# Performance work log

Hardware: AMD Instinct MI355X
Metric: run time of the kernel (lower is better)

Reference implementation:

```python
import jax, jax.numpy as jnp
import numpy as np

PC = (-51.2, -51.2, -5.0, 51.2, 51.2, 3.0)
BEV_H, BEV_W, BEV_Z = 50, 50, 4
NCAM, NUM_HEADS = 6, 8
EPS = 1e-5


def _layer_norm(x, g, b):
    m = jnp.mean(x, -1, keepdims=True)
    v = jnp.mean((x - m) ** 2, -1, keepdims=True)
    return (x - m) / jnp.sqrt(v + 1e-5) * g + b


def _grid_sample(imgs, pts):
    # imgs: (B,C,H,W); pts: (B,N,2) normalized coords; bilinear,
    # align_corners=False, zero padding (matches F.grid_sample defaults).
    B, C, H, W = imgs.shape
    def one(img, p):
        x = ((p[:, 0] + 1.0) * W - 1.0) * 0.5
        y = ((p[:, 1] + 1.0) * H - 1.0) * 0.5
        x0 = jnp.floor(x); y0 = jnp.floor(y)
        wx = x - x0; wy = y - y0
        def g(xi, yi):
            ok = (xi >= 0) & (xi < W) & (yi >= 0) & (yi < H)
            v = img[:, jnp.clip(yi, 0, H - 1).astype(jnp.int32),
                       jnp.clip(xi, 0, W - 1).astype(jnp.int32)]
            return v * ok[None, :]
        return (g(x0, y0) * (1 - wx) * (1 - wy) + g(x0 + 1, y0) * wx * (1 - wy)
                + g(x0, y0 + 1) * (1 - wx) * wy + g(x0 + 1, y0 + 1) * wx * wy)
    return jax.vmap(one)(imgs, pts)  # (B,C,N)


def _mha(q, kv, inW, inb, outW, outb):
    # torch nn.MultiheadAttention (batch_first)
    C = q.shape[-1]; d = C // NUM_HEADS
    B, Nq = q.shape[:2]; Nk = kv.shape[1]
    Q = q @ inW[:C].T + inb[:C]
    K = kv @ inW[C:2 * C].T + inb[C:2 * C]
    V = kv @ inW[2 * C:].T + inb[2 * C:]
    Qh = Q.reshape(B, Nq, NUM_HEADS, d).transpose(0, 2, 1, 3)
    Kh = K.reshape(B, Nk, NUM_HEADS, d).transpose(0, 2, 1, 3)
    Vh = V.reshape(B, Nk, NUM_HEADS, d).transpose(0, 2, 1, 3)
    s = jnp.einsum('bhqd,bhkd->bhqk', Qh, Kh) / float(np.sqrt(d))
    a = jax.nn.softmax(s, axis=-1)
    o = jnp.einsum('bhqk,bhkd->bhqd', a, Vh).transpose(0, 2, 1, 3).reshape(B, Nq, C)
    return o @ outW.T + outb


def _warp_prev(prev_bev, ego_motion):
    B, N, C = prev_bev.shape
    sp = prev_bev.transpose(0, 2, 1).reshape(B, C, BEV_H, BEV_W)
    tx = ego_motion[:, 0, 3]; ty = ego_motion[:, 1, 3]
    yaw = jnp.arctan2(ego_motion[:, 1, 0], ego_motion[:, 0, 0])
    dx = tx / ((PC[3] - PC[0]) / BEV_W) * 2.0 / BEV_W
    dy = ty / ((PC[4] - PC[1]) / BEV_H) * 2.0 / BEV_H
    c = jnp.cos(yaw); s = jnp.sin(yaw)
    theta = jnp.stack([jnp.stack([c, -s, dx], -1),
                       jnp.stack([s, c, dy], -1)], axis=1)  # (B,2,3)
    # F.affine_grid, align_corners=False: output-pixel-center base grid
    xs = (2.0 * jnp.arange(BEV_W) + 1.0) / BEV_W - 1.0
    ys = (2.0 * jnp.arange(BEV_H) + 1.0) / BEV_H - 1.0
    gx, gy = jnp.meshgrid(xs, ys)  # (H,W) each
    base = jnp.stack([gx, gy, jnp.ones_like(gx)], -1)  # (H,W,3)
    grid = jnp.einsum('bij,hwj->bhwi', theta, base).reshape(B, -1, 2)
    out = _grid_sample(sp, grid)  # (B,C,N)
    return out.transpose(0, 2, 1)


def _reference_points(B):
    ys = (jnp.arange(BEV_H, dtype=jnp.float32) + 0.5) / BEV_H
    xs = (jnp.arange(BEV_W, dtype=jnp.float32) + 0.5) / BEV_W
    ry, rx = jnp.meshgrid(ys, xs, indexing='ij')
    rx = rx.reshape(-1); ry = ry.reshape(-1)
    zs = (jnp.arange(BEV_Z, dtype=jnp.float32) + 0.5) / BEV_Z
    N = BEV_H * BEV_W
    ref = jnp.stack([jnp.broadcast_to(rx[:, None], (N, BEV_Z)),
                     jnp.broadcast_to(ry[:, None], (N, BEV_Z)),
                     jnp.broadcast_to(zs[None, :], (N, BEV_Z))], -1)
    return jnp.broadcast_to(ref[None], (B, N, BEV_Z, 3))  # (B,Nq,Z,3)


def _point_sampling(ref, img_feats, lidar2img):
    B, Nq, Zb, _ = ref.shape
    _, Ncam, C, Hf, Wf = img_feats.shape
    x = ref[..., 0] * (PC[3] - PC[0]) + PC[0]
    y = ref[..., 1] * (PC[4] - PC[1]) + PC[1]
    z = ref[..., 2] * (PC[5] - PC[2]) + PC[2]
    pts = jnp.stack([x, y, z, jnp.ones_like(x)], -1).reshape(B, 1, Nq * Zb, 4)
    pts = jnp.broadcast_to(pts, (B, Ncam, Nq * Zb, 4))
    cam = jnp.einsum('bnij,bnpj->bnpi', lidar2img, pts)
    depth = cam[..., 2]
    xy = cam[..., 0:2] / jnp.clip(depth, EPS)[..., None]
    gx = (xy[..., 0] / (Wf - 1) - 0.5) * 2.0
    gy = (xy[..., 1] / (Hf - 1) - 0.5) * 2.0
    valid = ((depth > EPS) & (gx > -1.0) & (gx < 1.0)
             & (gy > -1.0) & (gy < 1.0))  # (B,Ncam,Nq*Zb)
    grid = jnp.stack([gx, gy], -1).reshape(B * Ncam, Nq * Zb, 2)
    samp = _grid_sample(img_feats.reshape(B * Ncam, C, Hf, Wf), grid)
    samp = samp.reshape(B, Ncam, C, Nq, Zb) * valid.reshape(B, Ncam, 1, Nq, Zb)
    return jnp.nan_to_num(samp)


def _forward(query, prev_bev, img_feats, ego_motion, lidar2img,
             attn_w_W, attn_w_b, sca_out_W, sca_out_b,
             in_proj_W, in_proj_b, mha_out_W, mha_out_b,
             norm1_g, norm1_b, ffn_W1, ffn_b1, ffn_W2, ffn_b2,
             norm2_g, norm2_b):
    B, Nq, C = query.shape
    # Temporal self-attention with warped previous BEV
    aligned = _warp_prev(prev_bev, ego_motion)
    kv = jnp.concatenate([query, aligned], axis=1)
    attn = _mha(query, kv, in_proj_W, in_proj_b, mha_out_W, mha_out_b)
    q = _layer_norm(query + attn, norm1_g, norm1_b)
    # Spatial cross attention
    ref = _reference_points(B)
    samp = _point_sampling(ref, img_feats, lidar2img)  # (B,Ncam,C,Nq,Z)
    w = (q @ attn_w_W.T + attn_w_b).reshape(B, Nq, NCAM * BEV_Z)
    w = jax.nn.softmax(w, axis=-1).reshape(B, Nq, NCAM, BEV_Z)
    agg = jnp.einsum('bncqz,bqnz->bqc', samp, w)
    q = agg @ sca_out_W.T + sca_out_b + q
    # FFN (Linear -> ReLU -> Linear -> LayerNorm), residual outside
    h = jax.nn.relu(q @ ffn_W1.T + ffn_b1) @ ffn_W2.T + ffn_b2
    return q + _layer_norm(h, norm2_g, norm2_b)


def setup_inputs() -> dict:
    key = jax.random.key(0)
    ks = jax.random.split(key, 16)
    B, Nq, C, Hf, Wf = 1, BEV_H * BEV_W, 256, 28, 50
    s = 0.02
    d = {
        'query': jax.random.normal(ks[0], (B, Nq, C), jnp.float32),
        'prev_bev': jax.random.normal(ks[1], (B, Nq, C), jnp.float32),
        'img_feats': jax.random.normal(ks[2], (B, NCAM, C, Hf, Wf), jnp.float32),
        'ego_motion': jax.random.normal(ks[3], (B, 4, 4), jnp.float32),
        'lidar2img': jax.random.normal(ks[4], (B, NCAM, 4, 4), jnp.float32),
        'attn_w_W': jax.random.normal(ks[5], (NCAM * BEV_Z, C), jnp.float32) * s,
        'attn_w_b': jnp.zeros((NCAM * BEV_Z,), jnp.float32),
        'sca_out_W': jax.random.normal(ks[6], (C, C), jnp.float32) * s,
        'sca_out_b': jnp.zeros((C,), jnp.float32),
        'in_proj_W': jax.random.normal(ks[7], (3 * C, C), jnp.float32) * s,
        'in_proj_b': jnp.zeros((3 * C,), jnp.float32),
        'mha_out_W': jax.random.normal(ks[8], (C, C), jnp.float32) * s,
        'mha_out_b': jnp.zeros((C,), jnp.float32),
        'norm1_g': jnp.ones((C,), jnp.float32),
        'norm1_b': jnp.zeros((C,), jnp.float32),
        'ffn_W1': jax.random.normal(ks[9], (2 * C, C), jnp.float32) * s,
        'ffn_b1': jnp.zeros((2 * C,), jnp.float32),
        'ffn_W2': jax.random.normal(ks[10], (C, 2 * C), jnp.float32) * s,
        'ffn_b2': jnp.zeros((C,), jnp.float32),
        'norm2_g': jnp.ones((C,), jnp.float32),
        'norm2_b': jnp.zeros((C,), jnp.float32),
    }
    return d


def reference(query, prev_bev, img_feats, ego_motion, lidar2img,
              attn_w_W, attn_w_b, sca_out_W, sca_out_b,
              in_proj_W, in_proj_b, mha_out_W, mha_out_b,
              norm1_g, norm1_b, ffn_W1, ffn_b1, ffn_W2, ffn_b2,
              norm2_g, norm2_b):
    return _forward(query, prev_bev, img_feats, ego_motion, lidar2img,
                    attn_w_W, attn_w_b, sca_out_W, sca_out_b,
                    in_proj_W, in_proj_b, mha_out_W, mha_out_b,
                    norm1_g, norm1_b, ffn_W1, ffn_b1, ffn_W2, ffn_b2,
                    norm2_g, norm2_b)
```

## Files before the change

kernel.cpp:

```cpp
#include <hip/hip_runtime.h>
#include <hip/hip_bf16.h>
#include <math.h>

#define NQ   2500
#define CDIM 256
#define NKV  5000
#define NH   8
#define DH   32
#define SPLITS 10
#define KPS   500
#define FULLT 7
#define TILES 8
#define TAILNK 52

typedef __attribute__((ext_vector_type(8))) short bf16x8;
typedef __attribute__((ext_vector_type(4))) short short4v;
typedef __attribute__((ext_vector_type(4))) float f32x4;

#define MFMA __builtin_amdgcn_mfma_f32_16x16x32_bf16

__device__ __forceinline__ short f2bf(float f) {
  union { float f; unsigned u; } v; v.f = f;
  unsigned r = v.u + 0x7FFFu + ((v.u >> 16) & 1u);
  return (short)(r >> 16);
}
__device__ __forceinline__ float bf2f(unsigned short s) {
  union { unsigned u; float f; } x; x.u = ((unsigned)s) << 16; return x.f;
}
__device__ __forceinline__ unsigned pk_trunc(float a, float b) {
  union { float f; unsigned u; } x, y; x.f = a; y.f = b;
  return (y.u & 0xFFFF0000u) | (x.u >> 16);
}
__device__ __forceinline__ unsigned cvt_pk_bf16(float a, float b) {
  unsigned r;
  asm("v_cvt_pk_bf16_f32 %0, %1, %2" : "=v"(r) : "v"(a), "v"(b));
  return r;
}
__device__ __forceinline__ float exp2_fast(float x) {
  float r; asm("v_exp_f32 %0, %1" : "=v"(r) : "v"(x)); return r;
}

__global__ __launch_bounds__(256) void k_build_kv(
    const float* __restrict__ query, const float* __restrict__ prev,
    const float* __restrict__ ego, float* __restrict__ kv)
{
  int row = blockIdx.x, c = threadIdx.x;
  if (row < NQ) { kv[(size_t)row*CDIM + c] = query[(size_t)row*CDIM + c]; return; }
  int n = row - NQ;
  float txm = ego[3], tym = ego[7];
  float yaw = atan2f(ego[4], ego[0]);
  float cs = cosf(yaw), sn = sinf(yaw);
  float dx = txm * (1.f/51.2f), dy = tym * (1.f/51.2f);
  int i = n / 50, j = n % 50;
  float gx = (2.f*j + 1.f)*(1.f/50.f) - 1.f;
  float gy = (2.f*i + 1.f)*(1.f/50.f) - 1.f;
  float px = cs*gx - sn*gy + dx;
  float py = sn*gx + cs*gy + dy;
  float xf = ((px + 1.f)*50.f - 1.f)*0.5f;
  float yf = ((py + 1.f)*50.f - 1.f)*0.5f;
  float x0f = floorf(xf), y0f = floorf(yf);
  int x0 = (int)x0f, y0 = (int)y0f;
  float wx = xf - x0f, wy = yf - y0f;
  float v00 = (x0  >=0 && x0  <50 && y0  >=0 && y0  <50) ? prev[((size_t)(y0*50+x0      ))*CDIM + c] : 0.f;
  float v10 = (x0+1>=0 && x0+1<50 && y0  >=0 && y0  <50) ? prev[((size_t)(y0*50+x0+1    ))*CDIM + c] : 0.f;
  float v01 = (x0  >=0 && x0  <50 && y0+1>=0 && y0+1<50) ? prev[((size_t)((y0+1)*50+x0  ))*CDIM + c] : 0.f;
  float v11 = (x0+1>=0 && x0+1<50 && y0+1>=0 && y0+1<50) ? prev[((size_t)((y0+1)*50+x0+1))*CDIM + c] : 0.f;
  float v = (v00*(1.f-wx) + v10*wx)*(1.f-wy) + (v01*(1.f-wx) + v11*wx)*wy;
  kv[(size_t)row*CDIM + c] = v;
}

__global__ __launch_bounds__(256) void k_prep_w(
    const float* __restrict__ inW, const float* __restrict__ moW,
    const float* __restrict__ scaW, const float* __restrict__ fW1,
    const float* __restrict__ fW2, short* __restrict__ wf)
{
  const int id = blockIdx.x*256 + threadIdx.x;
  if (id >= 73728) return;
  const int s = id*8;
  const float* src; int off, K, obase;
  if      (s < 65536)  { src = inW;          off = s;          K = 256; obase = 0; }
  else if (s < 131072) { src = inW + 65536;  off = s - 65536;  K = 256; obase = 65536; }
  else if (s < 196608) { src = inW + 131072; off = s - 131072; K = 256; obase = 131072; }
  else if (s < 262144) { src = moW;          off = s - 196608; K = 256; obase = 196608; }
  else if (s < 327680) { src = scaW;         off = s - 262144; K = 256; obase = 262144; }
  else if (s < 458752) { src = fW1;          off = s - 327680; K = 256; obase = 327680; }
  else                 { src = fW2;          off = s - 458752; K = 512; obase = 458752; }
  const int n = off / K, k = off - n*K;
  short4v lo, hi;
  #pragma unroll
  for (int j = 0; j < 4; ++j) { lo[j] = f2bf(src[off+j]); hi[j] = f2bf(src[off+4+j]); }
  short* dst = wf + obase + (size_t)((n>>4)*(K>>3) + (k>>3))*128 + (n&15)*8;
  *(short4v*)dst = lo;
  *(short4v*)(dst+4) = hi;
}

__global__ __launch_bounds__(256) void k_repack_v(
    const short* __restrict__ VbfT, short* __restrict__ Vf)
{
  const int idx = blockIdx.x*256 + threadIdx.x;
  const int j    = idx & 7;
  const int lane = (idx >> 3) & 63;
  const int i    = (idx >> 9) & 1;
  const int kt2  = (idx >> 10) & 1;
  const int t    = (idx >> 11) & 7;
  const int h    = (idx >> 14) & 7;
  const int sp   = idx >> 17;
  const int gg = lane >> 4, cc = lane & 15;
  const int ko32 = ((j >> 2) << 4) | (gg << 2) | (j & 3);
  const int kin = t*64 + kt2*32 + ko32;
  const int d = i*16 + cc;
  short v = 0;
  if (kin < KPS) v = VbfT[(size_t)(h*32 + d)*NKV + sp*KPS + kin];
  Vf[idx] = v;
}

__global__ __launch_bounds__(256) void k_transpose_img(
    const float* __restrict__ img, unsigned short* __restrict__ imgT)
{
  int b = blockIdx.x;
  int n = b / 28, y = b % 28;
  int c = threadIdx.x;
  for (int x = 0; x < 50; ++x)
    imgT[((size_t)((n*28 + y)*50 + x))*CDIM + c] =
      (unsigned short)f2bf(img[((size_t)(n*CDIM + c)*28 + y)*50 + x]);
}

__global__ __launch_bounds__(256) void k_gemm(
    const float* __restrict__ A, const short* __restrict__ Wf,
    const float* __restrict__ bias, const float* __restrict__ res,
    float* __restrict__ C, short* __restrict__ Cb,
    int M, int N, int K, int relu, int mode, float scale)
{
  __shared__ short Abf[8][33][8];
  const int tid = threadIdx.x;
  const int lane = tid & 63, wid = tid >> 6;
  const int wm = wid >> 1, wn = wid & 1;
  const int g = lane >> 4, c = lane & 15;
  const int m0 = blockIdx.y << 5, n0 = blockIdx.x << 6;
  const int srow = tid >> 3, skq = tid & 7;
  const int kb8 = K >> 3;
  const short* wfa = Wf + (size_t)((n0 + wn*32) >> 4)      * kb8 * 128 + c*8;
  const short* wfb = Wf + (size_t)(((n0 + wn*32) >> 4) + 1) * kb8 * 128 + c*8;
  f32x4 acc0 = {0.f,0.f,0.f,0.f}, acc1 = acc0;
  const float4 z4 = make_float4(0.f,0.f,0.f,0.f);
  for (int k0 = 0; k0 < K; k0 += 64) {
    float4 fa0 = z4, fa1 = z4;
    if (m0 + srow < M) {
      const float* ap = A + (size_t)(m0+srow)*K + k0 + skq*8;
      fa0 = *(const float4*)ap; fa1 = *(const float4*)(ap+4);
    }
    __syncthreads();
    union { unsigned u[4]; bf16x8 v; } pa;
    pa.u[0] = cvt_pk_bf16(fa0.x, fa0.y);  pa.u[1] = cvt_pk_bf16(fa0.z, fa0.w);
    pa.u[2] = cvt_pk_bf16(fa1.x, fa1.y);  pa.u[3] = cvt_pk_bf16(fa1.z, fa1.w);
    *(bf16x8*)&Abf[skq][srow][0] = pa.v;
    __syncthreads();
    #pragma unroll
    for (int s = 0; s < 2; ++s) {
      const int kq = (k0 >> 3) + s*4 + g;
      const bf16x8 fA  = *(const bf16x8*)&Abf[s*4+g][wm*16 + c][0];
      const bf16x8 fW0 = *(const bf16x8*)(wfa + (size_t)kq*128);
      const bf16x8 fW1 = *(const bf16x8*)(wfb + (size_t)kq*128);
      acc0 = MFMA(fA, fW0, acc0, 0,0,0);
      acc1 = MFMA(fA, fW1, acc1, 0,0,0);
    }
  }
  const int nc0 = n0 + wn*32 + c, nc1 = nc0 + 16;
  const float b0v = bias[nc0], b1v = bias[nc1];
  #pragma unroll
  for (int r = 0; r < 4; ++r) {
    const int m = m0 + wm*16 + g*4 + r;
    if (m >= M) continue;
    float v0 = acc0[r] + b0v;
    float v1 = acc1[r] + b1v;
    if (mode == 0) {
      if (res) { v0 += res[(size_t)m*N + nc0]; v1 += res[(size_t)m*N + nc1]; }
      if (relu) { v0 = fmaxf(v0, 0.f); v1 = fmaxf(v1, 0.f); }
      C[(size_t)m*N + nc0] = v0;
      C[(size_t)m*N + nc1] = v1;
    } else if (mode == 1) {
      Cb[(size_t)m*N + nc0] = f2bf(v0*scale);
      Cb[(size_t)m*N + nc1] = f2bf(v1*scale);
    } else {
      Cb[(size_t)nc0*M + m] = f2bf(v0);
      Cb[(size_t)nc1*M + m] = f2bf(v1);
    }
  }
}

__device__ __forceinline__ void softmax_pv(
    f32x4 s0, f32x4 s1, f32x4 s2, f32x4 s3, bool tail, int g,
    float& m, float& l, f32x4& oA, f32x4& oB,
    bf16x8 A0lo, bf16x8 A0hi, bf16x8 A1lo, bf16x8 A1hi)
{
  float sv[16];
  #pragma unroll
  for (int r=0;r<4;++r){ sv[r]=s0[r]; sv[4+r]=s1[r]; sv[8+r]=s2[r]; sv[12+r]=s3[r]; }
  if (tail) {
    #pragma unroll
    for (int i=0;i<16;++i) {
      const int kl = (i>>2)*16 + g*4 + (i&3);
      if (kl >= TAILNK) sv[i] = -1e30f;
    }
  }
  float mx = fmaxf(fmaxf(fmaxf(sv[0],sv[1]),fmaxf(sv[2],sv[3])),
                   fmaxf(fmaxf(sv[4],sv[5]),fmaxf(sv[6],sv[7])));
  mx = fmaxf(mx, fmaxf(fmaxf(fmaxf(sv[8],sv[9]),fmaxf(sv[10],sv[11])),
                       fmaxf(fmaxf(sv[12],sv[13]),fmaxf(sv[14],sv[15]))));
  if (!__all(mx <= m + 8.f)) {
    float mm = fmaxf(mx, __shfl_xor(mx, 16));
    mm = fmaxf(mm, __shfl_xor(mm, 32));
    const float mn = fmaxf(m, mm);
    const float scl = exp2_fast(m - mn);
    m = mn;
    l *= scl;
    #pragma unroll
    for (int r=0;r<4;++r){ oA[r]*=scl; oB[r]*=scl; }
  }
  float p[16]; float ps = 0.f;
  #pragma unroll
  for (int i=0;i<16;++i){ p[i] = exp2_fast(sv[i]-m); ps += p[i]; }
  l += ps;
  union { unsigned u[4]; bf16x8 v; } b0, b1;
  #pragma unroll
  for (int i=0;i<4;++i) {
    b0.u[i] = pk_trunc(p[2*i],   p[2*i+1]);
    b1.u[i] = pk_trunc(p[8+2*i], p[8+2*i+1]);
  }
  oA = MFMA(A0lo, b0.v, oA, 0,0,0);
  oA = MFMA(A0hi, b1.v, oA, 0,0,0);
  oB = MFMA(A1lo, b0.v, oB, 0,0,0);
  oB = MFMA(A1hi, b1.v, oB, 0,0,0);
}

__global__ __launch_bounds__(64) void k_flash5(
    const short* __restrict__ Qbf, const short* __restrict__ Kbf,
    const short* __restrict__ Vf, short* __restrict__ opart,
    float* __restrict__ mlp)
{
  const int lane = threadIdx.x;
  const int g = lane >> 4, c = lane & 15;
  const int flat = blockIdx.x;
  const int p  = flat % 80;
  const int qb = flat / 80;
  const int h  = p & 7;
  const int sp = p >> 3;
  const int q0 = qb * 32;
  const int qa  = min(q0 +      c, NQ-1);
  const int qb2 = min(q0 + 16 + c, NQ-1);
  const bf16x8 qf0 = *(const bf16x8*)(Qbf + (size_t)qa *CDIM + h*DH + g*8);
  const bf16x8 qf1 = *(const bf16x8*)(Qbf + (size_t)qb2*CDIM + h*DH + g*8);
  const int kbase = sp*KPS;
  const size_t doff = (size_t)h*DH + g*8;
  const short* kbp = Kbf + (size_t)(kbase + c)*CDIM + doff;
  const short* vfp = Vf + (size_t)(sp*NH + h)*(TILES*2048) + lane*8;
  const f32x4 z = {0.f,0.f,0.f,0.f};
  f32x4 o00 = z, o01 = z, o10 = z, o11 = z;
  float m0v = -INFINITY, l0 = 0.f, m1v = -INFINITY, l1 = 0.f;

  bf16x8 kc0 = *(const bf16x8*)(kbp);
  bf16x8 kc1 = *(const bf16x8*)(kbp + (size_t)16*CDIM);
  bf16x8 kc2 = *(const bf16x8*)(kbp + (size_t)32*CDIM);
  bf16x8 kc3 = *(const bf16x8*)(kbp + (size_t)48*CDIM);

  #pragma unroll
  for (int t = 0; t < FULLT; ++t) {
    const int kt = t*64;
    const f32x4 s00 = MFMA(kc0, qf0, z, 0,0,0);
    const f32x4 s01 = MFMA(kc1, qf0, z, 0,0,0);
    const f32x4 s02 = MFMA(kc2, qf0, z, 0,0,0);
    const f32x4 s03 = MFMA(kc3, qf0, z, 0,0,0);
    const f32x4 s10 = MFMA(kc0, qf1, z, 0,0,0);
    const f32x4 s11 = MFMA(kc1, qf1, z, 0,0,0);
    const f32x4 s12 = MFMA(kc2, qf1, z, 0,0,0);
    const f32x4 s13 = MFMA(kc3, qf1, z, 0,0,0);
    if (t+1 < FULLT) {
      kc0 = *(const bf16x8*)(kbp + (size_t)(kt+64)*CDIM);
      kc1 = *(const bf16x8*)(kbp + (size_t)(kt+80)*CDIM);
      kc2 = *(const bf16x8*)(kbp + (size_t)(kt+96)*CDIM);
      kc3 = *(const bf16x8*)(kbp + (size_t)(kt+112)*CDIM);
    }
    const short* vt = vfp + (size_t)t*2048;
    const bf16x8 A0lo = *(const bf16x8*)(vt       );
    const bf16x8 A1lo = *(const bf16x8*)(vt +  512);
    const bf16x8 A0hi = *(const bf16x8*)(vt + 1024);
    const bf16x8 A1hi = *(const bf16x8*)(vt + 1536);
    softmax_pv(s00,s01,s02,s03, false, g, m0v, l0, o00, o01, A0lo, A0hi, A1lo, A1hi);
    softmax_pv(s10,s11,s12,s13, false, g, m1v, l1, o10, o11, A0lo, A0hi, A1lo, A1hi);
  }
  {
    const int kt = FULLT*64;
    const int ka0 = min(kbase + kt +      c, NKV-1);
    const int ka1 = min(kbase + kt + 16 + c, NKV-1);
    const int ka2 = min(kbase + kt + 32 + c, NKV-1);
    const int ka3 = min(kbase + kt + 48 + c, NKV-1);
    const bf16x8 kf0 = *(const bf16x8*)(Kbf + (size_t)ka0*CDIM + doff);
    const bf16x8 kf1 = *(const bf16x8*)(Kbf + (size_t)ka1*CDIM + doff);
    const bf16x8 kf2 = *(const bf16x8*)(Kbf + (size_t)ka2*CDIM + doff);
    const bf16x8 kf3 = *(const bf16x8*)(Kbf + (size_t)ka3*CDIM + doff);
    const f32x4 s00 = MFMA(kf0, qf0, z, 0,0,0);
    const f32x4 s01 = MFMA(kf1, qf0, z, 0,0,0);
    const f32x4 s02 = MFMA(kf2, qf0, z, 0,0,0);
    const f32x4 s03 = MFMA(kf3, qf0, z, 0,0,0);
    const f32x4 s10 = MFMA(kf0, qf1, z, 0,0,0);
    const f32x4 s11 = MFMA(kf1, qf1, z, 0,0,0);
    const f32x4 s12 = MFMA(kf2, qf1, z, 0,0,0);
    const f32x4 s13 = MFMA(kf3, qf1, z, 0,0,0);
    const short* vt = vfp + (size_t)FULLT*2048;
    const bf16x8 A0lo = *(const bf16x8*)(vt       );
    const bf16x8 A1lo = *(const bf16x8*)(vt +  512);
    const bf16x8 A0hi = *(const bf16x8*)(vt + 1024);
    const bf16x8 A1hi = *(const bf16x8*)(vt + 1536);
    softmax_pv(s00,s01,s02,s03, true, g, m0v, l0, o00, o01, A0lo, A0hi, A1lo, A1hi);
    softmax_pv(s10,s11,s12,s13, true, g, m1v, l1, o10, o11, A0lo, A0hi, A1lo, A1hi);
  }
  l0 += __shfl_xor(l0, 16); l0 += __shfl_xor(l0, 32);
  l1 += __shfl_xor(l1, 16); l1 += __shfl_xor(l1, 32);

  const size_t ob0 = (size_t)(sp*NH + h)*NQ;
  const int qw0 = q0 + c;
  if (qw0 < NQ) {
    const size_t b = (ob0 + qw0)*DH;
    #pragma unroll
    for (int r=0;r<4;++r) {
      opart[b +      g*4 + r] = f2bf(o00[r]);
      opart[b + 16 + g*4 + r] = f2bf(o01[r]);
    }
    if (g == 0) { mlp[(ob0 + qw0)*2] = m0v; mlp[(ob0 + qw0)*2+1] = l0; }
  }
  const int qw1 = q0 + 16 + c;
  if (qw1 < NQ) {
    const size_t b = (ob0 + qw1)*DH;
    #pragma unroll
    for (int r=0;r<4;++r) {
      opart[b +      g*4 + r] = f2bf(o10[r]);
      opart[b + 16 + g*4 + r] = f2bf(o11[r]);
    }
    if (g == 0) { mlp[(ob0 + qw1)*2] = m1v; mlp[(ob0 + qw1)*2+1] = l1; }
  }
}

__global__ __launch_bounds__(256) void k_combine(
    const short* __restrict__ opart, const float* __restrict__ mlp,
    float* __restrict__ attn)
{
  const int q = blockIdx.x, t = threadIdx.x;
  const int h = t >> 5, d = t & 31;
  float ms[SPLITS], ls[SPLITS];
  float mstar = -INFINITY;
  #pragma unroll
  for (int s = 0; s < SPLITS; ++s) {
    size_t b = (size_t)(s*NH + h)*NQ + q;
    ms[s] = mlp[b*2]; ls[s] = mlp[b*2+1];
    mstar = fmaxf(mstar, ms[s]);
  }
  float num = 0.f, den = 0.f;
  #pragma unroll
  for (int s = 0; s < SPLITS; ++s) {
    float e = exp2_fast(ms[s] - mstar);
    size_t b = (size_t)(s*NH + h)*NQ + q;
    num += bf2f((unsigned short)opart[b*DH + d])*e;
    den += ls[s]*e;
  }
  attn[(size_t)q*CDIM + t] = num/den;
}

__global__ __launch_bounds__(256) void k_ln(
    const float* __restrict__ x, const float* __restrict__ g,
    const float* __restrict__ b, const float* __restrict__ post_res,
    float* __restrict__ out)
{
  const int row = blockIdx.x, c = threadIdx.x;
  const size_t idx = (size_t)row*CDIM + c;
  const float v = x[idx];
  __shared__ float red[4];
  float s = v;
  #pragma unroll
  for (int m = 1; m < 64; m <<= 1) s += __shfl_xor(s, m);
  if ((c & 63) == 0) red[c >> 6] = s;
  __syncthreads();
  const float mean = (red[0]+red[1]+red[2]+red[3]) * (1.f/256.f);
  const float dv = v - mean;
  __syncthreads();
  float s2 = dv*dv;
  #pragma unroll
  for (int m = 1; m < 64; m <<= 1) s2 += __shfl_xor(s2, m);
  if ((c & 63) == 0) red[c >> 6] = s2;
  __syncthreads();
  const float var = (red[0]+red[1]+red[2]+red[3]) * (1.f/256.f);
  float o = dv * rsqrtf(var + 1e-5f) * g[c] + b[c];
  if (post_res) o += post_res[idx];
  out[idx] = o;
}

__global__ __launch_bounds__(256) void k_sample_agg(
    const float* __restrict__ q1, const unsigned short* __restrict__ imgT,
    const float* __restrict__ l2i, const float* __restrict__ awW,
    const float* __restrict__ awb, float* __restrict__ agg)
{
  const int q = blockIdx.x, tid = threadIdx.x;
  __shared__ float qrow[256];
  __shared__ float wl[24];
  __shared__ float fwx[24], fwy[24];
  __shared__ int iv[24], ix[24], iy[24];
  qrow[tid] = q1[(size_t)q*CDIM + tid];
  __syncthreads();
  if (tid < 192) {
    const int e = tid >> 3, s2 = tid & 7;
    float acc = 0.f;
    for (int c = s2; c < 256; c += 8) acc += qrow[c]*awW[e*256 + c];
    acc += __shfl_xor(acc,1);
    acc += __shfl_xor(acc,2);
    acc += __shfl_xor(acc,4);
    if (s2 == 0) wl[e] = acc + awb[e];
  }
  if (tid < 24) {
    const int e = tid, n = e >> 2, z = e & 3;
    const int iyq = q / 50, jxq = q % 50;
    const float rx = (jxq + 0.5f)*(1.f/50.f);
    const float ry = (iyq + 0.5f)*(1.f/50.f);
    const float rz = (z + 0.5f)*0.25f;
    const float X = rx*102.4f - 51.2f;
    const float Y = ry*102.4f - 51.2f;
    const float Z = rz*8.f - 5.f;
    const float* L = l2i + n*16;
    const float cx = L[0]*X + L[1]*Y + L[2]*Z  + L[3];
    const float cy = L[4]*X + L[5]*Y + L[6]*Z  + L[7];
    const float cd = L[8]*X + L[9]*Y + L[10]*Z + L[11];
    const float dn = fmaxf(cd, 1e-5f);
    const float u = cx/dn, vv = cy/dn;
    const float gx = (u*(1.f/49.f) - 0.5f)*2.f;
    const float gy = (vv*(1.f/27.f) - 0.5f)*2.f;
    const int ok = (cd > 1e-5f) && (gx > -1.f) && (gx < 1.f) && (gy > -1.f) && (gy < 1.f);
    const float xf = ((gx + 1.f)*50.f - 1.f)*0.5f;
    const float yf = ((gy + 1.f)*28.f - 1.f)*0.5f;
    const float x0f = floorf(xf), y0f = floorf(yf);
    iv[e] = ok; ix[e] = (int)x0f; iy[e] = (int)y0f;
    fwx[e] = xf - x0f; fwy[e] = yf - y0f;
  }
  __syncthreads();
  float mx = -INFINITY;
  #pragma unroll
  for (int e = 0; e < 24; ++e) mx = fmaxf(mx, wl[e]);
  float se = 0.f;
  #pragma unroll
  for (int e = 0; e < 24; ++e) se += __expf(wl[e]-mx);
  const float inv = 1.f/se;
  const int c = tid;
  float acc = 0.f;
  #pragma unroll
  for (int e = 0; e < 24; ++e) {
    if (!iv[e]) continue;
    const float w = __expf(wl[e]-mx)*inv;
    const int n = e >> 2;
    const int x0 = ix[e], y0 = iy[e];
    const float wx = fwx[e], wy = fwy[e];
    const size_t base = (size_t)(n*28)*50;
    float v00 = (x0  >=0 && x0  <50 && y0  >=0 && y0  <28) ? bf2f(imgT[((base + (size_t)y0*50     + x0  ))*CDIM + c]) : 0.f;
    float v10 = (x0+1>=0 && x0+1<50 && y0  >=0 && y0  <28) ? bf2f(imgT[((base + (size_t)y0*50     + x0+1))*CDIM + c]) : 0.f;
    float v01 = (x0  >=0 && x0  <50 && y0+1>=0 && y0+1<28) ? bf2f(imgT[((base + (size_t)(y0+1)*50 + x0  ))*CDIM + c]) : 0.f;
    float v11 = (x0+1>=0 && x0+1<50 && y0+1>=0 && y0+1<28) ? bf2f(imgT[((base + (size_t)(y0+1)*50 + x0+1))*CDIM + c]) : 0.f;
    acc += w * ((v00*(1.f-wx) + v10*wx)*(1.f-wy) + (v01*(1.f-wx) + v11*wx)*wy);
  }
  agg[(size_t)q*CDIM + c] = acc;
}

extern "C" void kernel_launch(void* const* d_in, const int* in_sizes, int n_in,
                              void* d_out, int out_size, void* d_ws, size_t ws_size,
                              hipStream_t stream)
{
  const float* query = (const float*)d_in[0];
  const float* prev  = (const float*)d_in[1];
  const float* img   = (const float*)d_in[2];
  const float* ego   = (const float*)d_in[3];
  const float* l2i   = (const float*)d_in[4];
  const float* awW   = (const float*)d_in[5];
  const float* awb   = (const float*)d_in[6];
  const float* scab  = (const float*)d_in[8];
  const float* inb   = (const float*)d_in[10];
  const float* mob   = (const float*)d_in[12];
  const float* n1g   = (const float*)d_in[13];
  const float* n1b   = (const float*)d_in[14];
  const float* fb1   = (const float*)d_in[16];
  const float* fb2   = (const float*)d_in[18];
  const float* n2g   = (const float*)d_in[19];
  const float* n2b   = (const float*)d_in[20];
  float* out = (float*)d_out;
  float* ws  = (float*)d_ws;

  float* kv    = ws;
  short* Qbf   = (short*)(ws + 1280000);
  short* Kbf   = (short*)(ws + 1600000);
  short* VbfT  = (short*)(ws + 2240000);
  short* Vf    = (short*)(ws + 2880000);
  short* opart = (short*)(ws + 3535360);
  float* mlp   = ws + 6735360;
  short* wf    = (short*)(ws + 7135360);
  unsigned short* imgT = (unsigned short*)(ws + 7430272);
  float* attn  = ws;
  float* tmp1  = ws +  640000;
  float* q1    = ws + 1280000;
  float* aggb  = ws + 1920000;
  float* q2    = ws + 2560000;
  float* hbuf  = ws + 3200000;
  float* h2    = ws + 4480000;

  const float qscale = 0.2550727452794943f;

  k_build_kv<<<NKV, 256, 0, stream>>>(query, prev, ego, kv);
  k_prep_w<<<288, 256, 0, stream>>>((const float*)d_in[9], (const float*)d_in[11],
                                    (const float*)d_in[7], (const float*)d_in[15],
                                    (const float*)d_in[17], wf);
  k_transpose_img<<<6*28, 256, 0, stream>>>(img, imgT);
  k_gemm<<<dim3(4,79),  256, 0, stream>>>(kv, wf,          inb,     nullptr, nullptr, Qbf,  NQ,  256, 256, 0, 1, qscale);
  k_gemm<<<dim3(4,157), 256, 0, stream>>>(kv, wf +  65536, inb+256, nullptr, nullptr, Kbf,  NKV, 256, 256, 0, 1, 1.0f);
  k_gemm<<<dim3(4,157), 256, 0, stream>>>(kv, wf + 131072, inb+512, nullptr, nullptr, VbfT, NKV, 256, 256, 0, 2, 1.0f);
  k_repack_v<<<5120, 256, 0, stream>>>(VbfT, Vf);
  k_flash5<<<79*80, 64, 0, stream>>>(Qbf, Kbf, Vf, opart, mlp);
  k_combine<<<NQ, 256, 0, stream>>>(opart, mlp, attn);
  k_gemm<<<dim3(4,79), 256, 0, stream>>>(attn, wf + 196608, mob, query, tmp1, nullptr, NQ, 256, 256, 0, 0, 1.0f);
  k_ln<<<NQ, 256, 0, stream>>>(tmp1, n1g, n1b, nullptr, q1);
  k_sample_agg<<<NQ, 256, 0, stream>>>(q1, imgT, l2i, awW, awb, aggb);
  k_gemm<<<dim3(4,79), 256, 0, stream>>>(aggb, wf + 262144, scab, q1, q2, nullptr, NQ, 256, 256, 0, 0, 1.0f);
  k_gemm<<<dim3(8,79), 256, 0, stream>>>(q2, wf + 327680, fb1, nullptr, hbuf, nullptr, NQ, 512, 256, 1, 0, 1.0f);
  k_gemm<<<dim3(4,79), 256, 0, stream>>>(hbuf, wf + 458752, fb2, nullptr, h2, nullptr, NQ, 256, 512, 0, 0, 1.0f);
  k_ln<<<NQ, 256, 0, stream>>>(h2, n2g, n2b, q2, out);
}
```

Baseline: 152.6 us.

## Fuse prep kernels and QKV GEMMs; compute softmax row sums via MFMA

Merges the kv build, image transpose and weight prep into one launch, and fuses the three Q/K/V projection GEMMs into a single grid that routes output columns to Q, K or transposed V. This cuts kernel launch count and gaps between launches. In the flash kernel, the per-lane exp-sum and cross-lane shuffle reduction are replaced by an MFMA against a ones vector, and P is packed with round-to-nearest conversion instead of truncation. The ones-MFMA adds matrix work per tile and sums the bf16-rounded probabilities, which slightly changes numerics. The fused QKV grid launches blocks past NQ for the Q columns, and these exit early.

```diff
diff --git a/kernel.cpp b/kernel.cpp
--- a/kernel.cpp
+++ b/kernel.cpp
@@ -27,10 +27,6 @@
 __device__ __forceinline__ float bf2f(unsigned short s) {
   union { unsigned u; float f; } x; x.u = ((unsigned)s) << 16; return x.f;
 }
-__device__ __forceinline__ unsigned pk_trunc(float a, float b) {
-  union { float f; unsigned u; } x, y; x.f = a; y.f = b;
-  return (y.u & 0xFFFF0000u) | (x.u >> 16);
-}
 __device__ __forceinline__ unsigned cvt_pk_bf16(float a, float b) {
   unsigned r;
   asm("v_cvt_pk_bf16_f32 %0, %1, %2" : "=v"(r) : "v"(a), "v"(b));
@@ -40,58 +36,129 @@
   float r; asm("v_exp_f32 %0, %1" : "=v"(r) : "v"(x)); return r;
 }
 
-__global__ __launch_bounds__(256) void k_build_kv(
+__global__ __launch_bounds__(256) void k_prep(
     const float* __restrict__ query, const float* __restrict__ prev,
-    const float* __restrict__ ego, float* __restrict__ kv)
-{
-  int row = blockIdx.x, c = threadIdx.x;
-  if (row < NQ) { kv[(size_t)row*CDIM + c] = query[(size_t)row*CDIM + c]; return; }
-  int n = row - NQ;
-  float txm = ego[3], tym = ego[7];
-  float yaw = atan2f(ego[4], ego[0]);
-  float cs = cosf(yaw), sn = sinf(yaw);
-  float dx = txm * (1.f/51.2f), dy = tym * (1.f/51.2f);
-  int i = n / 50, j = n % 50;
-  float gx = (2.f*j + 1.f)*(1.f/50.f) - 1.f;
-  float gy = (2.f*i + 1.f)*(1.f/50.f) - 1.f;
-  float px = cs*gx - sn*gy + dx;
-  float py = sn*gx + cs*gy + dy;
-  float xf = ((px + 1.f)*50.f - 1.f)*0.5f;
-  float yf = ((py + 1.f)*50.f - 1.f)*0.5f;
-  float x0f = floorf(xf), y0f = floorf(yf);
-  int x0 = (int)x0f, y0 = (int)y0f;
-  float wx = xf - x0f, wy = yf - y0f;
-  float v00 = (x0  >=0 && x0  <50 && y0  >=0 && y0  <50) ? prev[((size_t)(y0*50+x0      ))*CDIM + c] : 0.f;
-  float v10 = (x0+1>=0 && x0+1<50 && y0  >=0 && y0  <50) ? prev[((size_t)(y0*50+x0+1    ))*CDIM + c] : 0.f;
-  float v01 = (x0  >=0 && x0  <50 && y0+1>=0 && y0+1<50) ? prev[((size_t)((y0+1)*50+x0  ))*CDIM + c] : 0.f;
-  float v11 = (x0+1>=0 && x0+1<50 && y0+1>=0 && y0+1<50) ? prev[((size_t)((y0+1)*50+x0+1))*CDIM + c] : 0.f;
-  float v = (v00*(1.f-wx) + v10*wx)*(1.f-wy) + (v01*(1.f-wx) + v11*wx)*wy;
-  kv[(size_t)row*CDIM + c] = v;
-}
-
-__global__ __launch_bounds__(256) void k_prep_w(
+    const float* __restrict__ ego, float* __restrict__ kv,
+    const float* __restrict__ img, unsigned short* __restrict__ imgT,
     const float* __restrict__ inW, const float* __restrict__ moW,
     const float* __restrict__ scaW, const float* __restrict__ fW1,
     const float* __restrict__ fW2, short* __restrict__ wf)
 {
-  const int id = blockIdx.x*256 + threadIdx.x;
-  if (id >= 73728) return;
-  const int s = id*8;
-  const float* src; int off, K, obase;
-  if      (s < 65536)  { src = inW;          off = s;          K = 256; obase = 0; }
-  else if (s < 131072) { src = inW + 65536;  off = s - 65536;  K = 256; obase = 65536; }
-  else if (s < 196608) { src = inW + 131072; off = s - 131072; K = 256; obase = 131072; }
-  else if (s < 262144) { src = moW;          off = s - 196608; K = 256; obase = 196608; }
-  else if (s < 327680) { src = scaW;         off = s - 262144; K = 256; obase = 262144; }
-  else if (s < 458752) { src = fW1;          off = s - 327680; K = 256; obase = 327680; }
-  else                 { src = fW2;          off = s - 458752; K = 512; obase = 458752; }
-  const int n = off / K, k = off - n*K;
-  short4v lo, hi;
-  #pragma unroll
-  for (int j = 0; j < 4; ++j) { lo[j] = f2bf(src[off+j]); hi[j] = f2bf(src[off+4+j]); }
-  short* dst = wf + obase + (size_t)((n>>4)*(K>>3) + (k>>3))*128 + (n&15)*8;
-  *(short4v*)dst = lo;
-  *(short4v*)(dst+4) = hi;
+  const int gid = blockIdx.x, tid = threadIdx.x;
+  if (gid < NKV) {
+    const int row = gid, c = tid;
+    if (row < NQ) { kv[(size_t)row*CDIM + c] = query[(size_t)row*CDIM + c]; return; }
+    int n = row - NQ;
+    float txm = ego[3], tym = ego[7];
+    float yaw = atan2f(ego[4], ego[0]);
+    float cs = cosf(yaw), sn = sinf(yaw);
+    float dx = txm * (1.f/51.2f), dy = tym * (1.f/51.2f);
+    int i = n / 50, j = n % 50;
+    float gx = (2.f*j + 1.f)*(1.f/50.f) - 1.f;
+    float gy = (2.f*i + 1.f)*(1.f/50.f) - 1.f;
+    float px = cs*gx - sn*gy + dx;
+    float py = sn*gx + cs*gy + dy;
+    float xf = ((px + 1.f)*50.f - 1.f)*0.5f;
+    float yf = ((py + 1.f)*50.f - 1.f)*0.5f;
+    float x0f = floorf(xf), y0f = floorf(yf);
+    int x0 = (int)x0f, y0 = (int)y0f;
+    float wx = xf - x0f, wy = yf - y0f;
+    float v00 = (x0  >=0 && x0  <50 && y0  >=0 && y0  <50) ? prev[((size_t)(y0*50+x0      ))*CDIM + c] : 0.f;
+    float v10 = (x0+1>=0 && x0+1<50 && y0  >=0 && y0  <50) ? prev[((size_t)(y0*50+x0+1    ))*CDIM + c] : 0.f;
+    float v01 = (x0  >=0 && x0  <50 && y0+1>=0 && y0+1<50) ? prev[((size_t)((y0+1)*50+x0  ))*CDIM + c] : 0.f;
+    float v11 = (x0+1>=0 && x0+1<50 && y0+1>=0 && y0+1<50) ? prev[((size_t)((y0+1)*50+x0+1))*CDIM + c] : 0.f;
+    float v = (v00*(1.f-wx) + v10*wx)*(1.f-wy) + (v01*(1.f-wx) + v11*wx)*wy;
+    kv[(size_t)row*CDIM + c] = v;
+    return;
+  }
+  if (gid < NKV + 168) {
+    const int b = gid - NKV;
+    const int n = b / 28, y = b % 28;
+    const int c = tid;
+    for (int x = 0; x < 50; ++x)
+      imgT[((size_t)((n*28 + y)*50 + x))*CDIM + c] =
+        (unsigned short)f2bf(img[((size_t)(n*CDIM + c)*28 + y)*50 + x]);
+    return;
+  }
+  {
+    const int id = (gid - NKV - 168)*256 + tid;
+    if (id >= 73728) return;
+    const int s = id*8;
+    const float* src; int off, K, obase;
+    if      (s < 65536)  { src = inW;          off = s;          K = 256; obase = 0; }
+    else if (s < 131072) { src = inW + 65536;  off = s - 65536;  K = 256; obase = 65536; }
+    else if (s < 196608) { src = inW + 131072; off = s - 131072; K = 256; obase = 131072; }
+    else if (s < 262144) { src = moW;          off = s - 196608; K = 256; obase = 196608; }
+    else if (s < 327680) { src = scaW;         off = s - 262144; K = 256; obase = 262144; }
+    else if (s < 458752) { src = fW1;          off = s - 327680; K = 256; obase = 327680; }
+    else                 { src = fW2;          off = s - 458752; K = 512; obase = 458752; }
+    const int n = off / K, k = off - n*K;
+    short4v lo, hi;
+    #pragma unroll
+    for (int j = 0; j < 4; ++j) { lo[j] = f2bf(src[off+j]); hi[j] = f2bf(src[off+4+j]); }
+    short* dst = wf + obase + (size_t)((n>>4)*(K>>3) + (k>>3))*128 + (n&15)*8;
+    *(short4v*)dst = lo;
+    *(short4v*)(dst+4) = hi;
+  }
+}
+
+__global__ __launch_bounds__(256) void k_gemm_qkv(
+    const float* __restrict__ A, const short* __restrict__ Wf,
+    const float* __restrict__ bias, short* __restrict__ Qbf,
+    short* __restrict__ Kbf, short* __restrict__ VbfT, float qscale)
+{
+  __shared__ short Abf[8][33][8];
+  const int tid = threadIdx.x;
+  const int lane = tid & 63, wid = tid >> 6;
+  const int wm = wid >> 1, wn = wid & 1;
+  const int g = lane >> 4, c = lane & 15;
+  const int m0 = blockIdx.y << 5, n0 = blockIdx.x << 6;
+  if (n0 < 256 && m0 >= NQ) return;
+  const int srow = tid >> 3, skq = tid & 7;
+  const short* wfa = Wf + (size_t)((n0 + wn*32) >> 4)       * 32 * 128 + c*8;
+  const short* wfb = Wf + (size_t)(((n0 + wn*32) >> 4) + 1) * 32 * 128 + c*8;
+  f32x4 acc0 = {0.f,0.f,0.f,0.f}, acc1 = acc0;
+  for (int k0 = 0; k0 < 256; k0 += 64) {
+    const float* ap = A + (size_t)(m0+srow)*256 + k0 + skq*8;
+    const float4 fa0 = *(const float4*)ap;
+    const float4 fa1 = *(const float4*)(ap+4);
+    __syncthreads();
+    union { unsigned u[4]; bf16x8 v; } pa;
+    pa.u[0] = cvt_pk_bf16(fa0.x, fa0.y);  pa.u[1] = cvt_pk_bf16(fa0.z, fa0.w);
+    pa.u[2] = cvt_pk_bf16(fa1.x, fa1.y);  pa.u[3] = cvt_pk_bf16(fa1.z, fa1.w);
+    *(bf16x8*)&Abf[skq][srow][0] = pa.v;
+    __syncthreads();
+    #pragma unroll
+    for (int s = 0; s < 2; ++s) {
+      const int kq = (k0 >> 3) + s*4 + g;
+      const bf16x8 fA  = *(const bf16x8*)&Abf[s*4+g][wm*16 + c][0];
+      const bf16x8 fW0 = *(const bf16x8*)(wfa + (size_t)kq*128);
+      const bf16x8 fW1 = *(const bf16x8*)(wfb + (size_t)kq*128);
+      acc0 = MFMA(fA, fW0, acc0, 0,0,0);
+      acc1 = MFMA(fA, fW1, acc1, 0,0,0);
+    }
+  }
+  const int nc0 = n0 + wn*32 + c, nc1 = nc0 + 16;
+  const float b0v = bias[nc0], b1v = bias[nc1];
+  #pragma unroll
+  for (int r = 0; r < 4; ++r) {
+    const int m = m0 + wm*16 + g*4 + r;
+    if (m >= NKV) continue;
+    const float v0 = acc0[r] + b0v;
+    const float v1 = acc1[r] + b1v;
+    if (nc0 < 256) {
+      if (m < NQ) {
+        Qbf[(size_t)m*256 + nc0] = f2bf(v0*qscale);
+        Qbf[(size_t)m*256 + nc1] = f2bf(v1*qscale);
+      }
+    } else if (nc0 < 512) {
+      Kbf[(size_t)m*256 + nc0 - 256] = f2bf(v0);
+      Kbf[(size_t)m*256 + nc1 - 256] = f2bf(v1);
+    } else {
+      VbfT[(size_t)(nc0 - 512)*NKV + m] = f2bf(v0);
+      VbfT[(size_t)(nc1 - 512)*NKV + m] = f2bf(v1);
+    }
+  }
 }
 
 __global__ __launch_bounds__(256) void k_repack_v(
@@ -114,17 +181,6 @@
   Vf[idx] = v;
 }
 
-__global__ __launch_bounds__(256) void k_transpose_img(
-    const float* __restrict__ img, unsigned short* __restrict__ imgT)
-{
-  int b = blockIdx.x;
-  int n = b / 28, y = b % 28;
-  int c = threadIdx.x;
-  for (int x = 0; x < 50; ++x)
-    imgT[((size_t)((n*28 + y)*50 + x))*CDIM + c] =
-      (unsigned short)f2bf(img[((size_t)(n*CDIM + c)*28 + y)*50 + x]);
-}
-
 __global__ __launch_bounds__(256) void k_gemm(
     const float* __restrict__ A, const short* __restrict__ Wf,
     const float* __restrict__ bias, const float* __restrict__ res,
@@ -139,7 +195,7 @@
   const int m0 = blockIdx.y << 5, n0 = blockIdx.x << 6;
   const int srow = tid >> 3, skq = tid & 7;
   const int kb8 = K >> 3;
-  const short* wfa = Wf + (size_t)((n0 + wn*32) >> 4)      * kb8 * 128 + c*8;
+  const short* wfa = Wf + (size_t)((n0 + wn*32) >> 4)       * kb8 * 128 + c*8;
   const short* wfb = Wf + (size_t)(((n0 + wn*32) >> 4) + 1) * kb8 * 128 + c*8;
   f32x4 acc0 = {0.f,0.f,0.f,0.f}, acc1 = acc0;
   const float4 z4 = make_float4(0.f,0.f,0.f,0.f);
@@ -190,8 +246,8 @@
 
 __device__ __forceinline__ void softmax_pv(
     f32x4 s0, f32x4 s1, f32x4 s2, f32x4 s3, bool tail, int g,
-    float& m, float& l, f32x4& oA, f32x4& oB,
-    bf16x8 A0lo, bf16x8 A0hi, bf16x8 A1lo, bf16x8 A1hi)
+    float& m, f32x4& lacc, f32x4& oA, f32x4& oB,
+    bf16x8 A0lo, bf16x8 A0hi, bf16x8 A1lo, bf16x8 A1hi, bf16x8 ones)
 {
   float sv[16];
   #pragma unroll
@@ -203,37 +259,40 @@
       if (kl >= TAILNK) sv[i] = -1e30f;
     }
   }
-  float mx = fmaxf(fmaxf(fmaxf(sv[0],sv[1]),fmaxf(sv[2],sv[3])),
-                   fmaxf(fmaxf(sv[4],sv[5]),fmaxf(sv[6],sv[7])));
-  mx = fmaxf(mx, fmaxf(fmaxf(fmaxf(sv[8],sv[9]),fmaxf(sv[10],sv[11])),
-                       fmaxf(fmaxf(sv[12],sv[13]),fmaxf(sv[14],sv[15]))));
+  const float t0 = fmaxf(fmaxf(sv[0], sv[1]), sv[2]);
+  const float t1 = fmaxf(fmaxf(sv[3], sv[4]), sv[5]);
+  const float t2 = fmaxf(fmaxf(sv[6], sv[7]), sv[8]);
+  const float t3 = fmaxf(fmaxf(sv[9], sv[10]), sv[11]);
+  const float t4 = fmaxf(fmaxf(sv[12], sv[13]), sv[14]);
+  const float mx = fmaxf(fmaxf(fmaxf(t0, t1), t2), fmaxf(fmaxf(t3, t4), sv[15]));
   if (!__all(mx <= m + 8.f)) {
     float mm = fmaxf(mx, __shfl_xor(mx, 16));
     mm = fmaxf(mm, __shfl_xor(mm, 32));
     const float mn = fmaxf(m, mm);
     const float scl = exp2_fast(m - mn);
     m = mn;
-    l *= scl;
+    lacc[0] *= scl;
     #pragma unroll
     for (int r=0;r<4;++r){ oA[r]*=scl; oB[r]*=scl; }
   }
-  float p[16]; float ps = 0.f;
-  #pragma unroll
-  for (int i=0;i<16;++i){ p[i] = exp2_fast(sv[i]-m); ps += p[i]; }
-  l += ps;
+  float p[16];
+  #pragma unroll
+  for (int i=0;i<16;++i) p[i] = exp2_fast(sv[i]-m);
   union { unsigned u[4]; bf16x8 v; } b0, b1;
   #pragma unroll
   for (int i=0;i<4;++i) {
-    b0.u[i] = pk_trunc(p[2*i],   p[2*i+1]);
-    b1.u[i] = pk_trunc(p[8+2*i], p[8+2*i+1]);
+    b0.u[i] = cvt_pk_bf16(p[2*i],   p[2*i+1]);
+    b1.u[i] = cvt_pk_bf16(p[8+2*i], p[8+2*i+1]);
   }
   oA = MFMA(A0lo, b0.v, oA, 0,0,0);
   oA = MFMA(A0hi, b1.v, oA, 0,0,0);
   oB = MFMA(A1lo, b0.v, oB, 0,0,0);
   oB = MFMA(A1hi, b1.v, oB, 0,0,0);
-}
-
-__global__ __launch_bounds__(64) void k_flash5(
+  lacc = MFMA(ones, b0.v, lacc, 0,0,0);
+  lacc = MFMA(ones, b1.v, lacc, 0,0,0);
+}
+
+__global__ __launch_bounds__(64) void k_flash6(
     const short* __restrict__ Qbf, const short* __restrict__ Kbf,
     const short* __restrict__ Vf, short* __restrict__ opart,
     float* __restrict__ mlp)
@@ -250,13 +309,17 @@
   const int qb2 = min(q0 + 16 + c, NQ-1);
   const bf16x8 qf0 = *(const bf16x8*)(Qbf + (size_t)qa *CDIM + h*DH + g*8);
   const bf16x8 qf1 = *(const bf16x8*)(Qbf + (size_t)qb2*CDIM + h*DH + g*8);
+  bf16x8 ones;
+  #pragma unroll
+  for (int i=0;i<8;++i) ones[i] = (short)0x3F80;
   const int kbase = sp*KPS;
   const size_t doff = (size_t)h*DH + g*8;
   const short* kbp = Kbf + (size_t)(kbase + c)*CDIM + doff;
   const short* vfp = Vf + (size_t)(sp*NH + h)*(TILES*2048) + lane*8;
   const f32x4 z = {0.f,0.f,0.f,0.f};
   f32x4 o00 = z, o01 = z, o10 = z, o11 = z;
-  float m0v = -INFINITY, l0 = 0.f, m1v = -INFINITY, l1 = 0.f;
+  f32x4 lacc0 = z, lacc1 = z;
+  float m0v = -INFINITY, m1v = -INFINITY;
 
   bf16x8 kc0 = *(const bf16x8*)(kbp);
   bf16x8 kc1 = *(const bf16x8*)(kbp + (size_t)16*CDIM);
@@ -285,8 +348,8 @@
     const bf16x8 A1lo = *(const bf16x8*)(vt +  512);
     const bf16x8 A0hi = *(const bf16x8*)(vt + 1024);
     const bf16x8 A1hi = *(const bf16x8*)(vt + 1536);
-    softmax_pv(s00,s01,s02,s03, false, g, m0v, l0, o00, o01, A0lo, A0hi, A1lo, A1hi);
-    softmax_pv(s10,s11,s12,s13, false, g, m1v, l1, o10, o11, A0lo, A0hi, A1lo, A1hi);
+    softmax_pv(s00,s01,s02,s03, false, g, m0v, lacc0, o00, o01, A0lo, A0hi, A1lo, A1hi, ones);
+    softmax_pv(s10,s11,s12,s13, false, g, m1v, lacc1, o10, o11, A0lo, A0hi, A1lo, A1hi, ones);
   }
   {
     const int kt = FULLT*64;
@@ -311,12 +374,9 @@
     const bf16x8 A1lo = *(const bf16x8*)(vt +  512);
     const bf16x8 A0hi = *(const bf16x8*)(vt + 1024);
     const bf16x8 A1hi = *(const bf16x8*)(vt + 1536);
-    softmax_pv(s00,s01,s02,s03, true, g, m0v, l0, o00, o01, A0lo, A0hi, A1lo, A1hi);
-    softmax_pv(s10,s11,s12,s13, true, g, m1v, l1, o10, o11, A0lo, A0hi, A1lo, A1hi);
-  }
-  l0 += __shfl_xor(l0, 16); l0 += __shfl_xor(l0, 32);
-  l1 += __shfl_xor(l1, 16); l1 += __shfl_xor(l1, 32);
-
+    softmax_pv(s00,s01,s02,s03, true, g, m0v, lacc0, o00, o01, A0lo, A0hi, A1lo, A1hi, ones);
+    softmax_pv(s10,s11,s12,s13, true, g, m1v, lacc1, o10, o11, A0lo, A0hi, A1lo, A1hi, ones);
+  }
   const size_t ob0 = (size_t)(sp*NH + h)*NQ;
   const int qw0 = q0 + c;
   if (qw0 < NQ) {
@@ -326,7 +386,7 @@
       opart[b +      g*4 + r] = f2bf(o00[r]);
       opart[b + 16 + g*4 + r] = f2bf(o01[r]);
     }
-    if (g == 0) { mlp[(ob0 + qw0)*2] = m0v; mlp[(ob0 + qw0)*2+1] = l0; }
+    if (g == 0) { mlp[(ob0 + qw0)*2] = m0v; mlp[(ob0 + qw0)*2+1] = lacc0[0]; }
   }
   const int qw1 = q0 + 16 + c;
   if (qw1 < NQ) {
@@ -336,7 +396,7 @@
       opart[b +      g*4 + r] = f2bf(o10[r]);
       opart[b + 16 + g*4 + r] = f2bf(o11[r]);
     }
-    if (g == 0) { mlp[(ob0 + qw1)*2] = m1v; mlp[(ob0 + qw1)*2+1] = l1; }
+    if (g == 0) { mlp[(ob0 + qw1)*2] = m1v; mlp[(ob0 + qw1)*2+1] = lacc1[0]; }
   }
 }
 
@@ -507,16 +567,13 @@
 
   const float qscale = 0.2550727452794943f;
 
-  k_build_kv<<<NKV, 256, 0, stream>>>(query, prev, ego, kv);
-  k_prep_w<<<288, 256, 0, stream>>>((const float*)d_in[9], (const float*)d_in[11],
-                                    (const float*)d_in[7], (const float*)d_in[15],
-                                    (const float*)d_in[17], wf);
-  k_transpose_img<<<6*28, 256, 0, stream>>>(img, imgT);
-  k_gemm<<<dim3(4,79),  256, 0, stream>>>(kv, wf,          inb,     nullptr, nullptr, Qbf,  NQ,  256, 256, 0, 1, qscale);
-  k_gemm<<<dim3(4,157), 256, 0, stream>>>(kv, wf +  65536, inb+256, nullptr, nullptr, Kbf,  NKV, 256, 256, 0, 1, 1.0f);
-  k_gemm<<<dim3(4,157), 256, 0, stream>>>(kv, wf + 131072, inb+512, nullptr, nullptr, VbfT, NKV, 256, 256, 0, 2, 1.0f);
+  k_prep<<<5456, 256, 0, stream>>>(query, prev, ego, kv, img, imgT,
+                                   (const float*)d_in[9], (const float*)d_in[11],
+                                   (const float*)d_in[7], (const float*)d_in[15],
+                                   (const float*)d_in[17], wf);
+  k_gemm_qkv<<<dim3(12,157), 256, 0, stream>>>(kv, wf, inb, Qbf, Kbf, VbfT, qscale);
   k_repack_v<<<5120, 256, 0, stream>>>(VbfT, Vf);
-  k_flash5<<<79*80, 64, 0, stream>>>(Qbf, Kbf, Vf, opart, mlp);
+  k_flash6<<<79*80, 64, 0, stream>>>(Qbf, Kbf, Vf, opart, mlp);
   k_combine<<<NQ, 256, 0, stream>>>(opart, mlp, attn);
   k_gemm<<<dim3(4,79), 256, 0, stream>>>(attn, wf + 196608, mob, query, tmp1, nullptr, NQ, 256, 256, 0, 0, 1.0f);
   k_ln<<<NQ, 256, 0, stream>>>(tmp1, n1g, n1b, nullptr, q1);
```

After: 141.1 us. -7.5%, faster.
